# Optimization experiments

Hardware: AMD Instinct MI355X
Metric: run time of the kernel (lower is better)

The kernel has to match this reference:

```python
import jax, jax.numpy as jnp
import numpy as np

N_VARS = 2048
BATCH = 1024


def encode_input(pos):
    # pos: [n_vars, batch] -> [2*n_vars + 2, batch]
    # row 0 = 0, row 1 = 1, even rows >=2 = pos, odd rows >=3 = 1 - pos
    n = pos.shape[0]
    out = jnp.zeros((2 * n + 2,) + pos.shape[1:], dtype=pos.dtype)
    out = out.at[1].set(1.0)
    out = out.at[2::2].set(pos)
    out = out.at[3::2].set(1.0 - pos)
    return out


def setup_inputs() -> dict:
    key = jax.random.key(0)
    k0, k1, k2, k3, k4 = jax.random.split(key, 5)
    x = jax.random.uniform(k0, (N_VARS, BATCH), dtype=jnp.float32)
    idx0 = jax.random.randint(k1, (32768, 2), 0, 2 * N_VARS + 2, dtype=jnp.int32)
    idx1 = jax.random.randint(k2, (16384, 2), 0, 32768, dtype=jnp.int32)
    idx2 = jax.random.randint(k3, (8192, 2), 0, 16384, dtype=jnp.int32)
    idx3 = jax.random.randint(k4, (4096, 2), 0, 8192, dtype=jnp.int32)
    return {"x": x, "idx0": idx0, "idx1": idx1, "idx2": idx2, "idx3": idx3}


def reference(x, idx0, idx1, idx2, idx3):
    h = encode_input(x)                  # [2*n_vars+2, B]
    h = h[idx0].prod(axis=1)             # ProductLayer: [32768, B]
    h = h[idx1].sum(axis=1)              # SumLayer:     [16384, B]
    h = h[idx2].prod(axis=1)             # ProductLayer: [8192, B]
    h = h[idx3].sum(axis=1)              # SumLayer:     [4096, B]
    return h
```

## Files before the change

### kernel.cpp

```cpp
#include <hip/hip_runtime.h>
#include <hip/hip_fp16.h>

#define BATCH  1024
#define NVARS  2048
#define N_OUT  4096

#define W32BYTES (NVARS * 64)
#define NW32     (BATCH / 32)

typedef float f32x4 __attribute__((ext_vector_type(4)));
typedef unsigned u32x4 __attribute__((ext_vector_type(4)));

__device__ __forceinline__ __half2 u2h2(unsigned u) {
    union { unsigned u; __half2 h; } c; c.u = u; return c.h;
}
__device__ __forceinline__ unsigned h22u(__half2 h) {
    union { unsigned u; __half2 h; } c; c.h = h; return c.u;
}
__device__ __forceinline__ void sel2sc(unsigned sel, unsigned& s, unsigned& c) {
    c = (sel & 1u) ? 0x3C003C00u : 0u;
    s = (sel == 2u) ? 0x3C003C00u : (sel == 3u) ? 0xBC00BC00u : 0u;
}

__global__ __launch_bounds__(256) void prep_kernel(
    const float* __restrict__ x,
    const int2* __restrict__ idx0,
    const int2* __restrict__ idx1,
    const int2* __restrict__ idx2,
    const int2* __restrict__ idx3,
    unsigned* __restrict__ T,
    char* __restrict__ xh2)
{
    __shared__ char tile[64 * 272];

    const int bid = blockIdx.x;
    const int tid = threadIdx.x;
    const int rt  = bid >> 3;
    const int ct  = bid & 7;
    const int r0  = rt * 64;

    if (bid < 16) {
        const int i = bid * 256 + tid;
        int2 p3 = idx3[i];
        int n = 0;
        #pragma unroll
        for (int t = 0; t < 2; ++t) {
            int2 p2 = idx2[t ? p3.y : p3.x];
            #pragma unroll
            for (int u = 0; u < 2; ++u) {
                int2 p1 = idx1[u ? p2.y : p2.x];
                #pragma unroll
                for (int v = 0; v < 2; ++v) {
                    int2 p0 = idx0[v ? p1.y : p1.x];
                    unsigned w = 0;
                    #pragma unroll
                    for (int e = 0; e < 2; ++e) {
                        int k = e ? p0.y : p0.x;
                        unsigned code;
                        if (k < 2) code = (unsigned)k << 11;
                        else       code = ((2u + (k & 1)) << 11) | ((unsigned)(k - 2) >> 1);
                        w |= code << (16 * e);
                    }
                    __builtin_nontemporal_store(w, &T[(size_t)i * 8 + n]);
                    ++n;
                }
            }
        }
    }

    {
        const int r_l = tid >> 5;
        const int c4  = tid & 31;
        #pragma unroll
        for (int q = 0; q < 8; ++q) {
            const int rr = q * 8 + r_l;
            float4 v = ((const float4*)x)[(size_t)(r0 + rr) * 256 + ct * 32 + c4];
            unsigned h0 = h22u(__floats2half2_rn(v.x, v.y));
            unsigned h1 = h22u(__floats2half2_rn(v.z, v.w));
            unsigned* p = (unsigned*)(tile + rr * 272 + c4 * 8);
            p[0] = h0; p[1] = h1;
        }
    }
    __syncthreads();

    {
        const int wl = tid & 3;
        const int r2 = tid >> 2;
        #pragma unroll
        for (int g = 0; g < 4; ++g) {
            u32x4 v = *reinterpret_cast<const u32x4*>(tile + r2 * 272 + g * 64 + wl * 16);
            const int w32 = ct * 4 + g;
            __builtin_nontemporal_store(
                v, reinterpret_cast<u32x4*>(
                       xh2 + (size_t)w32 * W32BYTES + (r0 + r2) * 64 + wl * 16));
        }
    }
}

__global__ __launch_bounds__(1024) void knowledge_main(
    const char* __restrict__ xh2,
    const uint4* __restrict__ T4,
    float* __restrict__ out)
{
    __shared__ char lds[131072];

    const int bx   = blockIdx.x;
    const int tid  = threadIdx.x;
    const int xcd  = bx & 7;
    const int slot = bx >> 3;
    const int w    = xcd * 4 + (slot & 3);
    const int chunk= slot >> 2;

    {
        const char* src = xh2 + (size_t)w * W32BYTES;
        #pragma unroll
        for (int it = 0; it < 8; ++it) {
            const int u = it * 1024 + tid;
            *(uint4*)(lds + u * 16) = *(const uint4*)(src + u * 16);
        }
    }
    __syncthreads();

    const int cg  = tid & 3;
    const int ol  = tid >> 2;
    const int cgb = cg * 16;

    int o = chunk * 512 + ol;
    uint4 t0 = T4[(size_t)o * 2];
    uint4 t1 = T4[(size_t)o * 2 + 1];

    #pragma unroll 1
    for (int pass = 0; pass < 2; ++pass) {
        const unsigned tw[8] = {t0.x, t0.y, t0.z, t0.w, t1.x, t1.y, t1.z, t1.w};

        if (pass == 0) {
            t0 = T4[(size_t)(o + 256) * 2];
            t1 = T4[(size_t)(o + 256) * 2 + 1];
        }

        float accf[8];
        #pragma unroll
        for (int k = 0; k < 8; ++k) accf[k] = 0.f;

        #pragma unroll
        for (int a3 = 0; a3 < 2; ++a3) {
            __half2 prod2[4];
            #pragma unroll
            for (int a2 = 0; a2 < 2; ++a2) {
                __half2 sum1[4];
                #pragma unroll
                for (int a1 = 0; a1 < 2; ++a1) {
                    const int m = a3 * 4 + a2 * 2 + a1;
                    const unsigned wv = tw[m];
                    uint4 A = *(const uint4*)(lds + ((wv & 0x7FFu) << 6) + cgb);
                    uint4 B = *(const uint4*)(lds + (((wv >> 16) & 0x7FFu) << 6) + cgb);
                    unsigned sa, ca, sb, cb;
                    sel2sc((wv >> 11) & 3u, sa, ca);
                    sel2sc((wv >> 27) & 3u, sb, cb);
                    const unsigned aw[4] = {A.x, A.y, A.z, A.w};
                    const unsigned bw[4] = {B.x, B.y, B.z, B.w};
                    #pragma unroll
                    for (int k = 0; k < 4; ++k) {
                        __half2 va = __hfma2(u2h2(aw[k]), u2h2(sa), u2h2(ca));
                        __half2 vb = __hfma2(u2h2(bw[k]), u2h2(sb), u2h2(cb));
                        __half2 pr = __hmul2(va, vb);
                        sum1[k] = (a1 == 0) ? pr : __hadd2(sum1[k], pr);
                    }
                }
                #pragma unroll
                for (int k = 0; k < 4; ++k)
                    prod2[k] = (a2 == 0) ? sum1[k] : __hmul2(prod2[k], sum1[k]);
            }
            #pragma unroll
            for (int k = 0; k < 4; ++k) {
                float2 pf = __half22float2(prod2[k]);
                accf[2 * k]     += pf.x;
                accf[2 * k + 1] += pf.y;
            }
        }

        float* dst = out + (size_t)o * BATCH + w * 32 + cg * 8;
        f32x4 o0 = {accf[0], accf[1], accf[2], accf[3]};
        f32x4 o1 = {accf[4], accf[5], accf[6], accf[7]};
        __builtin_nontemporal_store(o0, reinterpret_cast<f32x4*>(dst));
        __builtin_nontemporal_store(o1, reinterpret_cast<f32x4*>(dst) + 1);

        o += 256;
    }
}

__device__ __forceinline__ float Hval(int k, const float* __restrict__ x, int b) {
    if (k < 2) return (float)k;
    float v = x[((k - 2) >> 1) * BATCH + b];
    return (k & 1) ? 1.0f - v : v;
}

__global__ __launch_bounds__(256) void knowledge_fused_kernel(
    const float* __restrict__ x,
    const int2* __restrict__ idx0,
    const int2* __restrict__ idx1,
    const int2* __restrict__ idx2,
    const int2* __restrict__ idx3,
    float* __restrict__ out)
{
    const int i = blockIdx.x;
    const int b = blockIdx.y * blockDim.x + threadIdx.x;
    const int2 p3 = idx3[i];
    float acc3 = 0.0f;
    #pragma unroll
    for (int t = 0; t < 2; ++t) {
        const int2 p2 = idx2[t ? p3.y : p3.x];
        float prod2 = 1.0f;
        #pragma unroll
        for (int u = 0; u < 2; ++u) {
            const int2 p1 = idx1[u ? p2.y : p2.x];
            float sum1 = 0.0f;
            #pragma unroll
            for (int v = 0; v < 2; ++v) {
                const int2 p0 = idx0[v ? p1.y : p1.x];
                sum1 += Hval(p0.x, x, b) * Hval(p0.y, x, b);
            }
            prod2 *= sum1;
        }
        acc3 += prod2;
    }
    out[(size_t)i * BATCH + b] = acc3;
}

extern "C" void kernel_launch(void* const* d_in, const int* in_sizes, int n_in,
                              void* d_out, int out_size, void* d_ws, size_t ws_size,
                              hipStream_t stream) {
    const float* x    = (const float*)d_in[0];
    const int2*  idx0 = (const int2*)d_in[1];
    const int2*  idx1 = (const int2*)d_in[2];
    const int2*  idx2 = (const int2*)d_in[3];
    const int2*  idx3 = (const int2*)d_in[4];
    float* out = (float*)d_out;

    const size_t t_bytes   = (size_t)N_OUT * 8 * sizeof(unsigned);
    const size_t xh2_bytes = (size_t)NW32 * W32BYTES;
    if (ws_size >= t_bytes + xh2_bytes) {
        unsigned* T   = (unsigned*)d_ws;
        char*     xh2 = (char*)d_ws + t_bytes;
        prep_kernel<<<256, 256, 0, stream>>>(x, idx0, idx1, idx2, idx3, T, xh2);
        knowledge_main<<<256, 1024, 0, stream>>>(xh2, (const uint4*)T, out);
    } else {
        dim3 grid(N_OUT, BATCH / 256);
        knowledge_fused_kernel<<<grid, 256, 0, stream>>>(x, idx0, idx1, idx2, idx3, out);
    }
}
```

Measured before the change: 18.60 us.

## Convert x to fp16 inside main kernel, drop the transposed half workspace

The prep kernel no longer transposes and converts x into a per-32-column fp16 workspace. Each main-kernel block now reads its 32-column slice of the fp32 x directly, converts it to half and writes it into LDS, and the prep kernel shrinks to 16 blocks that only flatten the index tree. This removes a round trip of x through global memory and makes the first kernel much shorter. In exchange, every main block does strided 128-byte-per-row fp32 reads, so x is read as fp32 8 times across the blocks sharing a column slice.

```diff
diff --git a/kernel.cpp b/kernel.cpp
--- a/kernel.cpp
+++ b/kernel.cpp
@@ -5,11 +5,7 @@
 #define NVARS  2048
 #define N_OUT  4096
 
-#define W32BYTES (NVARS * 64)
-#define NW32     (BATCH / 32)
-
 typedef float f32x4 __attribute__((ext_vector_type(4)));
-typedef unsigned u32x4 __attribute__((ext_vector_type(4)));
 
 __device__ __forceinline__ __half2 u2h2(unsigned u) {
     union { unsigned u; __half2 h; } c; c.u = u; return c.h;
@@ -22,101 +18,66 @@
     s = (sel == 2u) ? 0x3C003C00u : (sel == 3u) ? 0xBC00BC00u : 0u;
 }
 
-__global__ __launch_bounds__(256) void prep_kernel(
-    const float* __restrict__ x,
+__global__ __launch_bounds__(256) void tflat_kernel(
     const int2* __restrict__ idx0,
     const int2* __restrict__ idx1,
     const int2* __restrict__ idx2,
     const int2* __restrict__ idx3,
-    unsigned* __restrict__ T,
-    char* __restrict__ xh2)
+    unsigned* __restrict__ T)
 {
-    __shared__ char tile[64 * 272];
-
-    const int bid = blockIdx.x;
-    const int tid = threadIdx.x;
-    const int rt  = bid >> 3;
-    const int ct  = bid & 7;
-    const int r0  = rt * 64;
-
-    if (bid < 16) {
-        const int i = bid * 256 + tid;
-        int2 p3 = idx3[i];
-        int n = 0;
-        #pragma unroll
-        for (int t = 0; t < 2; ++t) {
-            int2 p2 = idx2[t ? p3.y : p3.x];
-            #pragma unroll
-            for (int u = 0; u < 2; ++u) {
-                int2 p1 = idx1[u ? p2.y : p2.x];
+    const int i = blockIdx.x * 256 + threadIdx.x;
+    int2 p3 = idx3[i];
+    int n = 0;
+    #pragma unroll
+    for (int t = 0; t < 2; ++t) {
+        int2 p2 = idx2[t ? p3.y : p3.x];
+        #pragma unroll
+        for (int u = 0; u < 2; ++u) {
+            int2 p1 = idx1[u ? p2.y : p2.x];
+            #pragma unroll
+            for (int v = 0; v < 2; ++v) {
+                int2 p0 = idx0[v ? p1.y : p1.x];
+                unsigned w = 0;
                 #pragma unroll
-                for (int v = 0; v < 2; ++v) {
-                    int2 p0 = idx0[v ? p1.y : p1.x];
-                    unsigned w = 0;
-                    #pragma unroll
-                    for (int e = 0; e < 2; ++e) {
-                        int k = e ? p0.y : p0.x;
-                        unsigned code;
-                        if (k < 2) code = (unsigned)k << 11;
-                        else       code = ((2u + (k & 1)) << 11) | ((unsigned)(k - 2) >> 1);
-                        w |= code << (16 * e);
-                    }
-                    __builtin_nontemporal_store(w, &T[(size_t)i * 8 + n]);
-                    ++n;
+                for (int e = 0; e < 2; ++e) {
+                    int k = e ? p0.y : p0.x;
+                    unsigned code;
+                    if (k < 2) code = (unsigned)k << 11;
+                    else       code = ((2u + (k & 1)) << 11) | ((unsigned)(k - 2) >> 1);
+                    w |= code << (16 * e);
                 }
-            }
-        }
-    }
-
-    {
-        const int r_l = tid >> 5;
-        const int c4  = tid & 31;
-        #pragma unroll
-        for (int q = 0; q < 8; ++q) {
-            const int rr = q * 8 + r_l;
-            float4 v = ((const float4*)x)[(size_t)(r0 + rr) * 256 + ct * 32 + c4];
-            unsigned h0 = h22u(__floats2half2_rn(v.x, v.y));
-            unsigned h1 = h22u(__floats2half2_rn(v.z, v.w));
-            unsigned* p = (unsigned*)(tile + rr * 272 + c4 * 8);
-            p[0] = h0; p[1] = h1;
-        }
-    }
-    __syncthreads();
-
-    {
-        const int wl = tid & 3;
-        const int r2 = tid >> 2;
-        #pragma unroll
-        for (int g = 0; g < 4; ++g) {
-            u32x4 v = *reinterpret_cast<const u32x4*>(tile + r2 * 272 + g * 64 + wl * 16);
-            const int w32 = ct * 4 + g;
-            __builtin_nontemporal_store(
-                v, reinterpret_cast<u32x4*>(
-                       xh2 + (size_t)w32 * W32BYTES + (r0 + r2) * 64 + wl * 16));
+                __builtin_nontemporal_store(w, &T[(size_t)i * 8 + n]);
+                ++n;
+            }
         }
     }
 }
 
 __global__ __launch_bounds__(1024) void knowledge_main(
-    const char* __restrict__ xh2,
+    const float* __restrict__ x,
     const uint4* __restrict__ T4,
     float* __restrict__ out)
 {
     __shared__ char lds[131072];
 
-    const int bx   = blockIdx.x;
-    const int tid  = threadIdx.x;
-    const int xcd  = bx & 7;
-    const int slot = bx >> 3;
-    const int w    = xcd * 4 + (slot & 3);
-    const int chunk= slot >> 2;
+    const int bx    = blockIdx.x;
+    const int tid   = threadIdx.x;
+    const int xcd   = bx & 7;
+    const int slot  = bx >> 3;
+    const int w     = xcd * 4 + (slot & 3);
+    const int chunk = slot >> 2;
 
     {
-        const char* src = xh2 + (size_t)w * W32BYTES;
-        #pragma unroll
-        for (int it = 0; it < 8; ++it) {
+        const float4* x4 = (const float4*)x;
+        #pragma unroll
+        for (int it = 0; it < 16; ++it) {
             const int u = it * 1024 + tid;
-            *(uint4*)(lds + u * 16) = *(const uint4*)(src + u * 16);
+            const int r = u >> 3, p = u & 7;
+            float4 v = x4[(size_t)r * 256 + w * 8 + p];
+            uint2 d;
+            d.x = h22u(__floats2half2_rn(v.x, v.y));
+            d.y = h22u(__floats2half2_rn(v.z, v.w));
+            *(uint2*)(lds + r * 64 + p * 8) = d;
         }
     }
     __syncthreads();
@@ -237,13 +198,11 @@
     const int2*  idx3 = (const int2*)d_in[4];
     float* out = (float*)d_out;
 
-    const size_t t_bytes   = (size_t)N_OUT * 8 * sizeof(unsigned);
-    const size_t xh2_bytes = (size_t)NW32 * W32BYTES;
-    if (ws_size >= t_bytes + xh2_bytes) {
-        unsigned* T   = (unsigned*)d_ws;
-        char*     xh2 = (char*)d_ws + t_bytes;
-        prep_kernel<<<256, 256, 0, stream>>>(x, idx0, idx1, idx2, idx3, T, xh2);
-        knowledge_main<<<256, 1024, 0, stream>>>(xh2, (const uint4*)T, out);
+    const size_t t_bytes = (size_t)N_OUT * 8 * sizeof(unsigned);
+    if (ws_size >= t_bytes) {
+        unsigned* T = (unsigned*)d_ws;
+        tflat_kernel<<<16, 256, 0, stream>>>(idx0, idx1, idx2, idx3, T);
+        knowledge_main<<<256, 1024, 0, stream>>>(x, (const uint4*)T, out);
     } else {
         dim3 grid(N_OUT, BATCH / 256);
         knowledge_fused_kernel<<<grid, 256, 0, stream>>>(x, idx0, idx1, idx2, idx3, out);
```

Result: slower. 19.95 us (+7.2%).
